# Performance work log

Hardware: AMD Instinct MI355X
Metric: run time of the kernel (lower is better)

The kernel has to match this reference:

```python
import jax, jax.numpy as jnp
import numpy as np

N_NODES = 100000
N_EDGES = 1600000
N_FEAT = 16
HIDDEN = 128
N_GRAPHS = 512


def setup_inputs() -> dict:
    key = jax.random.key(0)
    ks = jax.random.split(key, 9)
    x = jax.random.normal(ks[0], (N_NODES, N_FEAT), dtype=jnp.float32)
    edge_index = jax.random.randint(ks[1], (2, N_EDGES), 0, N_NODES, dtype=jnp.int64)
    batch = jnp.sort(jax.random.randint(ks[2], (N_NODES,), 0, N_GRAPHS, dtype=jnp.int64))
    s1 = 1.0 / np.sqrt(N_FEAT)
    s2 = 1.0 / np.sqrt(HIDDEN)
    W1 = jax.random.uniform(ks[3], (N_FEAT, HIDDEN), jnp.float32, -s1, s1)
    b1 = jax.random.uniform(ks[4], (HIDDEN,), jnp.float32, -s1, s1)
    W2 = jax.random.uniform(ks[5], (HIDDEN, HIDDEN), jnp.float32, -s2, s2)
    b2 = jax.random.uniform(ks[6], (HIDDEN,), jnp.float32, -s2, s2)
    Wl = jax.random.uniform(ks[7], (HIDDEN, 1), jnp.float32, -s2, s2)
    bl = jax.random.uniform(ks[8], (1,), jnp.float32, -s2, s2)
    return {"x": x, "edge_index": edge_index, "batch": batch,
            "W1": W1, "b1": b1, "W2": W2, "b2": b2, "Wl": Wl, "bl": bl}


def _gcn_conv(x, W, b, src, dst, n_nodes):
    # PyG GCNConv: h = x @ W; add self-loops; sym-normalized scatter-add; + bias
    h = x @ W  # [N, H]
    deg = jnp.zeros((n_nodes,), h.dtype).at[dst].add(1.0) + 1.0  # self-loop adds 1
    dinv = jax.lax.rsqrt(deg)  # deg >= 1, safe
    norm = dinv[src] * dinv[dst]  # [E]
    out = jnp.zeros_like(h).at[dst].add(h[src] * norm[:, None])
    out = out + h * (dinv * dinv)[:, None]  # self-loop term
    return out + b


def reference(x, edge_index, batch, W1, b1, W2, b2, Wl, bl):
    src, dst = edge_index[0], edge_index[1]
    n = x.shape[0]
    h = jax.nn.relu(_gcn_conv(x, W1, b1, src, dst, n))
    h = jax.nn.relu(_gcn_conv(h, W2, b2, src, dst, n))
    # global_mean_pool over graphs
    sums = jax.ops.segment_sum(h, batch, num_segments=N_GRAPHS)
    counts = jax.ops.segment_sum(jnp.ones((n,), h.dtype), batch, num_segments=N_GRAPHS)
    pooled = sums / jnp.maximum(counts, 1.0)[:, None]  # [G, H]
    return (pooled @ Wl + bl).squeeze(-1)  # [G]
```

## Files before the change

kernel.cpp:

```cpp
#include <hip/hip_runtime.h>
#include <hip/hip_bf16.h>

#define N_NODES 100000
#define N_EDGES 1600000
#define N_FEAT  16
#define HIDDEN  128
#define N_GRAPHS 512
#define CAP     64
#define NBKT    782
#define BN      128
#define CAPB    2560
#define EPB     4000

typedef unsigned short ushort_t;
typedef unsigned char uchar_t;
typedef short v8s __attribute__((ext_vector_type(8)));
typedef float v4f __attribute__((ext_vector_type(4)));
typedef float v2f __attribute__((ext_vector_type(2)));

#if defined(__has_builtin)
#if __has_builtin(__builtin_amdgcn_cvt_pk_f32_fp8) && __has_builtin(__builtin_amdgcn_cvt_pk_fp8_f32)
#define FP8_HW 1
#endif
#endif

__device__ __forceinline__ ushort_t f2bf(float f) {
    __hip_bfloat16 b = __float2bfloat16(f);
    return *(ushort_t*)&b;
}
__device__ __forceinline__ float bf_lo(unsigned u) {
    union { unsigned i; float f; } c; c.i = u << 16; return c.f;
}
__device__ __forceinline__ float bf_hi(unsigned u) {
    union { unsigned i; float f; } c; c.i = u & 0xffff0000u; return c.f;
}

__device__ __forceinline__ uchar_t f2fp8(float v) {
#ifdef FP8_HW
    return (uchar_t)(__builtin_amdgcn_cvt_pk_fp8_f32(v, 0.0f, 0, false) & 0xff);
#else
    if (!(v > 0.0f)) return 0;
    if (v >= 448.0f) return 0x7E;
    union { float f; unsigned u; } c; c.f = v;
    int e = ((c.u >> 23) & 255) - 127;
    unsigned m = c.u & 0x7fffff;
    if (e >= -6) {
        unsigned mm = m >> 20;
        unsigned rest = m & 0xfffff;
        if (rest > 0x80000u || (rest == 0x80000u && (mm & 1))) mm++;
        if (mm == 8) { mm = 0; e++; if (e > 8) return 0x7E; }
        return (uchar_t)(((e + 7) << 3) | mm);
    } else {
        int q = (int)(v * 512.0f + 0.5f);
        if (q > 7) q = 7;
        return (uchar_t)q;
    }
#endif
}

#ifndef FP8_HW
__device__ __forceinline__ float fp8d(unsigned b) {
    b &= 0xff;
    unsigned s = b >> 7, e = (b >> 3) & 15, m = b & 7;
    float v;
    if (e == 0) v = (float)m * (1.0f / 512.0f);
    else { union { unsigned u; float f; } c; c.u = ((e + 120u) << 23) | (m << 20); v = c.f; }
    return s ? -v : v;
}
#endif

__device__ __forceinline__ void fp8x8_acc(uint2 v, float& a0, float& a1, float& a2, float& a3,
                                          float& a4, float& a5, float& a6, float& a7) {
#ifdef FP8_HW
    v2f p0 = __builtin_amdgcn_cvt_pk_f32_fp8(v.x, false);
    v2f p1 = __builtin_amdgcn_cvt_pk_f32_fp8(v.x, true);
    v2f p2 = __builtin_amdgcn_cvt_pk_f32_fp8(v.y, false);
    v2f p3 = __builtin_amdgcn_cvt_pk_f32_fp8(v.y, true);
    a0 += p0[0]; a1 += p0[1]; a2 += p1[0]; a3 += p1[1];
    a4 += p2[0]; a5 += p2[1]; a6 += p3[0]; a7 += p3[1];
#else
    a0 += fp8d(v.x);       a1 += fp8d(v.x >> 8);
    a2 += fp8d(v.x >> 16); a3 += fp8d(v.x >> 24);
    a4 += fp8d(v.y);       a5 += fp8d(v.y >> 8);
    a6 += fp8d(v.y >> 16); a7 += fp8d(v.y >> 24);
#endif
}


__global__ __launch_bounds__(256) void k_part(const int* __restrict__ src,
                                              const int* __restrict__ dst,
                                              int* __restrict__ bcnt,
                                              int* __restrict__ ebuf,
                                              const float* __restrict__ W2,
                                              ushort_t* __restrict__ Bp) {
    int tid = threadIdx.x;

    if (blockIdx.x >= N_EDGES / EPB) {
        int idx = (blockIdx.x - N_EDGES / EPB) * 256 + tid;
        int j = idx & 7;
        int lane = (idx >> 3) & 63;
        int nt = (idx >> 9) & 7;
        int kt = idx >> 12;
        int k = kt * 32 + (lane >> 4) * 8 + j;
        int n = nt * 16 + (lane & 15);
        Bp[idx] = f2bf(W2[k * HIDDEN + n]);
        return;
    }

    __shared__ int h[NBKT];
    __shared__ int base[NBKT];
    __shared__ int r[NBKT];
    int e0 = blockIdx.x * EPB;

    for (int i = tid; i < NBKT; i += 256) { h[i] = 0; r[i] = 0; }
    __syncthreads();

    int nloc = (tid < EPB - 15 * 256) ? 16 : 15;
    int v[16], bb[16];
    #pragma unroll
    for (int k = 0; k < 16; ++k) {
        if (k < nloc) {
            int i = e0 + tid + k * 256;
            int s = src[i], d = dst[i];
            bb[k] = d >> 7;
            v[k] = s | ((d & 127) << 17);
            atomicAdd(&h[bb[k]], 1);
        }
    }
    __syncthreads();

    for (int i = tid; i < NBKT; i += 256)
        base[i] = atomicAdd(&bcnt[i], h[i]);
    __syncthreads();

    #pragma unroll
    for (int k = 0; k < 16; ++k) {
        if (k < nloc) {
            int b = bb[k];
            int pos = base[b] + atomicAdd(&r[b], 1);
            if (pos < CAPB) ebuf[b * CAPB + pos] = v[k];
        }
    }
}


__global__ __launch_bounds__(256) void k_fill(const int* __restrict__ bcnt,
                                              const int* __restrict__ ebuf,
                                              const float* __restrict__ x,
                                              int* __restrict__ esrc64,
                                              int* __restrict__ cnt,
                                              float* __restrict__ dinv,
                                              ushort_t* __restrict__ xb,
                                              uchar_t* __restrict__ h1q) {
    __shared__ int lcnt[BN];
    int tid = threadIdx.x;
    int b = blockIdx.x;
    int node0 = b << 7;

    if (tid < BN) lcnt[tid] = 0;
    __syncthreads();

    int nE = bcnt[b]; nE = nE > CAPB ? CAPB : nE;
    const int* eb = ebuf + b * CAPB;
    for (int i = tid; i < nE; i += 256) {
        int v = eb[i];
        int dl = v >> 17;
        int p = atomicAdd(&lcnt[dl], 1);
        if (p < CAP) esrc64[((node0 + dl) << 6) + p] = v & 0x1FFFF;
    }
    __syncthreads();

    if (tid < BN) {
        int node = node0 + tid;
        if (node < N_NODES) {
            int c = lcnt[tid];
            cnt[node] = c;
            dinv[node] = rsqrtf((float)c + 1.0f);
            int cc = c > CAP ? CAP : c;
            int pad = (cc + 7) & ~7;
            for (int p = cc; p < pad; ++p)
                esrc64[(node << 6) + p] = N_NODES;
        }
    }

    for (int i = tid; i < BN * N_FEAT; i += 256) {
        int nl = i >> 4;
        int node = node0 + nl;
        if (node < N_NODES) {
            float di = rsqrtf((float)lcnt[nl] + 1.0f);
            xb[node * N_FEAT + (i & 15)] = f2bf(x[node * N_FEAT + (i & 15)] * di);
        }
    }

    if (b == 0) {
        if (tid < N_FEAT) xb[N_NODES * N_FEAT + tid] = 0;
        if (tid < HIDDEN) h1q[(size_t)N_NODES * HIDDEN + tid] = 0;
    }
}


__global__ __launch_bounds__(256) void k_agg1f(const int* __restrict__ cnt,
                                               const int* __restrict__ esrc64,
                                               const float* __restrict__ dinv,
                                               const ushort_t* __restrict__ xb,
                                               const float* __restrict__ W1,
                                               const float* __restrict__ b1,
                                               uchar_t* __restrict__ h1q) {
    __shared__ float sw[N_FEAT * HIDDEN];
    __shared__ float sx[32][20];
    __shared__ float sdd[32];
    int tid = threadIdx.x;
    for (int i = tid; i < N_FEAT * HIDDEN; i += 256) sw[i] = W1[i];

    int wv = tid >> 6;
    int sub = (tid >> 3) & 7;
    int l8 = tid & 7;
    int nl = wv * 8 + sub;
    int node = blockIdx.x * 32 + nl;
    const unsigned* xr = (const unsigned*)xb;

    int deg = cnt[node]; deg = deg > CAP ? CAP : deg;
    int deg8 = (deg + 7) & ~7;
    int base = node << 6;
    float dd = dinv[node];

    float a0 = 0.0f, a1 = 0.0f;
    for (int j = 0; j < deg8; j += 8) {
        int4 ia = *(const int4*)(esrc64 + base + j);
        int4 ib = *(const int4*)(esrc64 + base + j + 4);
        unsigned u0 = xr[(unsigned)ia.x * 8 + l8];
        unsigned u1 = xr[(unsigned)ia.y * 8 + l8];
        unsigned u2 = xr[(unsigned)ia.z * 8 + l8];
        unsigned u3 = xr[(unsigned)ia.w * 8 + l8];
        unsigned u4 = xr[(unsigned)ib.x * 8 + l8];
        unsigned u5 = xr[(unsigned)ib.y * 8 + l8];
        unsigned u6 = xr[(unsigned)ib.z * 8 + l8];
        unsigned u7 = xr[(unsigned)ib.w * 8 + l8];
        a0 += bf_lo(u0) + bf_lo(u1) + bf_lo(u2) + bf_lo(u3)
            + bf_lo(u4) + bf_lo(u5) + bf_lo(u6) + bf_lo(u7);
        a1 += bf_hi(u0) + bf_hi(u1) + bf_hi(u2) + bf_hi(u3)
            + bf_hi(u4) + bf_hi(u5) + bf_hi(u6) + bf_hi(u7);
    }
    unsigned su = xr[(unsigned)node * 8 + l8];
    a0 = (a0 + bf_lo(su)) * dd;
    a1 = (a1 + bf_hi(su)) * dd;

    sx[nl][2 * l8] = a0;
    sx[nl][2 * l8 + 1] = a1;
    if (l8 == 0) sdd[nl] = dd;
    __syncthreads();

    int f = tid & 127, half = tid >> 7;
    float bias = b1[f];
    float acc[16];
    #pragma unroll
    for (int n = 0; n < 16; ++n) acc[n] = bias;
    #pragma unroll
    for (int k4 = 0; k4 < 4; ++k4) {
        float w0 = sw[(k4 * 4 + 0) * HIDDEN + f];
        float w1 = sw[(k4 * 4 + 1) * HIDDEN + f];
        float w2 = sw[(k4 * 4 + 2) * HIDDEN + f];
        float w3 = sw[(k4 * 4 + 3) * HIDDEN + f];
        #pragma unroll
        for (int n = 0; n < 16; ++n) {
            float4 xv = *(const float4*)(&sx[half * 16 + n][k4 * 4]);
            acc[n] += xv.x * w0 + xv.y * w1 + xv.z * w2 + xv.w * w3;
        }
    }
    int n0 = blockIdx.x * 32 + half * 16;
    #pragma unroll
    for (int n = 0; n < 16; ++n)
        h1q[(size_t)(n0 + n) * HIDDEN + f] =
            f2fp8(sdd[half * 16 + n] * fmaxf(acc[n], 0.0f));
}


__global__ __launch_bounds__(256) void k_l2(const int* __restrict__ cnt,
                                            const int* __restrict__ esrc64,
                                            const float* __restrict__ dinv,
                                            const uchar_t* __restrict__ h1q,
                                            const ushort_t* __restrict__ Bp,
                                            const float* __restrict__ b2,
                                            const float* __restrict__ Wl,
                                            float* __restrict__ snode) {
    __shared__ ushort_t sA[64 * 132];
    int tid = threadIdx.x;
    int wv = tid >> 6, lane = tid & 63;
    int l16 = lane & 15, q = lane >> 4;
    int node0 = blockIdx.x * 64;
    const uint2* h2 = (const uint2*)h1q;

    for (int p = 0; p < 4; ++p) {
        int nl = wv * 16 + p * 4 + q;
        int nodeIdx = node0 + nl;
        int node = nodeIdx < N_NODES ? nodeIdx : 0;
        int deg = cnt[node]; deg = deg > CAP ? CAP : deg;
        int deg8 = (deg + 7) & ~7;
        int base = node << 6;
        float dd = dinv[node];
        float a0 = 0.f, a1 = 0.f, a2 = 0.f, a3 = 0.f;
        float a4 = 0.f, a5 = 0.f, a6 = 0.f, a7 = 0.f;
        uint2 sv = h2[(unsigned)node * 16 + l16];
        fp8x8_acc(sv, a0, a1, a2, a3, a4, a5, a6, a7);

        int4 ia = *(const int4*)(esrc64 + base);
        int4 ib = *(const int4*)(esrc64 + base + 4);
        for (int j = 0; j < deg8; j += 8) {
            int jn = j + 8; jn = jn > CAP - 8 ? CAP - 8 : jn;
            int4 ian = *(const int4*)(esrc64 + base + jn);
            int4 ibn = *(const int4*)(esrc64 + base + jn + 4);
            uint2 v0 = h2[(unsigned)ia.x * 16 + l16];
            uint2 v1 = h2[(unsigned)ia.y * 16 + l16];
            uint2 v2 = h2[(unsigned)ia.z * 16 + l16];
            uint2 v3 = h2[(unsigned)ia.w * 16 + l16];
            uint2 v4 = h2[(unsigned)ib.x * 16 + l16];
            uint2 v5 = h2[(unsigned)ib.y * 16 + l16];
            uint2 v6 = h2[(unsigned)ib.z * 16 + l16];
            uint2 v7 = h2[(unsigned)ib.w * 16 + l16];
            fp8x8_acc(v0, a0, a1, a2, a3, a4, a5, a6, a7);
            fp8x8_acc(v1, a0, a1, a2, a3, a4, a5, a6, a7);
            fp8x8_acc(v2, a0, a1, a2, a3, a4, a5, a6, a7);
            fp8x8_acc(v3, a0, a1, a2, a3, a4, a5, a6, a7);
            fp8x8_acc(v4, a0, a1, a2, a3, a4, a5, a6, a7);
            fp8x8_acc(v5, a0, a1, a2, a3, a4, a5, a6, a7);
            fp8x8_acc(v6, a0, a1, a2, a3, a4, a5, a6, a7);
            fp8x8_acc(v7, a0, a1, a2, a3, a4, a5, a6, a7);
            ia = ian; ib = ibn;
        }
        unsigned r0 = (unsigned)f2bf(a0 * dd) | ((unsigned)f2bf(a1 * dd) << 16);
        unsigned r1 = (unsigned)f2bf(a2 * dd) | ((unsigned)f2bf(a3 * dd) << 16);
        unsigned r2 = (unsigned)f2bf(a4 * dd) | ((unsigned)f2bf(a5 * dd) << 16);
        unsigned r3 = (unsigned)f2bf(a6 * dd) | ((unsigned)f2bf(a7 * dd) << 16);
        uint2 w0; w0.x = r0; w0.y = r1;
        uint2 w1; w1.x = r2; w1.y = r3;
        *(uint2*)(&sA[nl * 132 + l16 * 8]) = w0;
        *(uint2*)(&sA[nl * 132 + l16 * 8 + 4]) = w1;
    }

    int m = lane & 15, quad = lane >> 4;
    const ushort_t* arow = &sA[(wv * 16 + m) * 132];

    v4f acc[8];
    #pragma unroll
    for (int nt = 0; nt < 8; ++nt) acc[nt] = (v4f){0.f, 0.f, 0.f, 0.f};

    #pragma unroll
    for (int kt = 0; kt < 4; ++kt) {
        union { v8s v; ushort4 q[2]; } au;
        au.q[0] = *(const ushort4*)(arow + kt * 32 + quad * 8);
        au.q[1] = *(const ushort4*)(arow + kt * 32 + quad * 8 + 4);
        #pragma unroll
        for (int nt = 0; nt < 8; ++nt) {
            v8s b = *(const v8s*)(Bp + ((kt * 8 + nt) * 64 + lane) * 8);
            acc[nt] = __builtin_amdgcn_mfma_f32_16x16x32_bf16(au.v, b, acc[nt], 0, 0, 0);
        }
    }

    float part[4] = {0, 0, 0, 0};
    #pragma unroll
    for (int nt = 0; nt < 8; ++nt) {
        float bb = b2[nt * 16 + m];
        float wl = Wl[nt * 16 + m];
        #pragma unroll
        for (int reg = 0; reg < 4; ++reg)
            part[reg] += fmaxf(acc[nt][reg] + bb, 0.0f) * wl;
    }
    int node0b = node0 + wv * 16;
    #pragma unroll
    for (int reg = 0; reg < 4; ++reg) {
        float p = part[reg];
        p += __shfl_xor(p, 1, 64);
        p += __shfl_xor(p, 2, 64);
        p += __shfl_xor(p, 4, 64);
        p += __shfl_xor(p, 8, 64);
        int node = node0b + quad * 4 + reg;
        if (m == 0 && node < N_NODES) snode[node] = p;
    }
}


__global__ __launch_bounds__(256) void k_pool(const float* __restrict__ snode,
                                              const int* __restrict__ batch,
                                              const float* __restrict__ bl,
                                              float* __restrict__ out) {
    int g = blockIdx.x;
    int tid = threadIdx.x;
    __shared__ float sred[4];

    int lo = 0, hi = N_NODES;
    while (lo < hi) { int mid = (lo + hi) >> 1; if (batch[mid] < g) lo = mid + 1; else hi = mid; }
    int start = lo;
    hi = N_NODES;
    while (lo < hi) { int mid = (lo + hi) >> 1; if (batch[mid] < g + 1) lo = mid + 1; else hi = mid; }
    int end = lo;

    float acc = 0.0f;
    for (int n = start + tid; n < end; n += 256) acc += snode[n];

    #pragma unroll
    for (int off = 32; off; off >>= 1) acc += __shfl_down(acc, off, 64);
    int wave = tid >> 6, lane = tid & 63;
    if (lane == 0) sred[wave] = acc;
    __syncthreads();
    if (tid == 0) {
        float s = sred[0] + sred[1] + sred[2] + sred[3];
        float cnt = (float)(end - start);
        out[g] = s / fmaxf(cnt, 1.0f) + bl[0];
    }
}


extern "C" void kernel_launch(void* const* d_in, const int* in_sizes, int n_in,
                              void* d_out, int out_size, void* d_ws, size_t ws_size,
                              hipStream_t stream) {
    const float* x    = (const float*)d_in[0];
    const int*   src  = (const int*)d_in[1];
    const int*   dst  = src + N_EDGES;
    const int*   batch= (const int*)d_in[2];
    const float* W1   = (const float*)d_in[3];
    const float* b1   = (const float*)d_in[4];
    const float* W2   = (const float*)d_in[5];
    const float* b2   = (const float*)d_in[6];
    const float* Wl   = (const float*)d_in[7];
    const float* bl   = (const float*)d_in[8];
    float* out = (float*)d_out;

    char* w = (char*)d_ws;
    size_t off = 0;
    auto alloc = [&](size_t bytes) { char* p = w + off; off = (off + bytes + 255) & ~(size_t)255; return p; };

    uchar_t* h1q   = (uchar_t*)alloc((size_t)(N_NODES + 1) * HIDDEN);
    int*   ebuf    = (int*)alloc((size_t)NBKT * CAPB * 4);
    ushort_t* xb   = (ushort_t*)alloc((size_t)(N_NODES + 1) * N_FEAT * 2);
    float* dinv    = (float*)alloc(N_NODES * 4);
    float* snode   = (float*)alloc(N_NODES * 4);
    int*   cnt     = (int*)alloc(N_NODES * 4);
    int*   esrc64  = (int*)alloc((size_t)N_NODES * CAP * 4);
    ushort_t* Bp   = (ushort_t*)alloc(16384 * 2);
    int*   bcnt    = (int*)alloc(NBKT * 4);

    hipMemsetAsync(bcnt, 0, NBKT * sizeof(int), stream);
    k_part<<<N_EDGES / EPB + 64, 256, 0, stream>>>(src, dst, bcnt, ebuf, W2, Bp);
    k_fill<<<NBKT, 256, 0, stream>>>(bcnt, ebuf, x, esrc64, cnt, dinv, xb, h1q);

    k_agg1f<<<N_NODES / 32, 256, 0, stream>>>(cnt, esrc64, dinv, xb, W1, b1, h1q);

    k_l2<<<(N_NODES + 63) / 64, 256, 0, stream>>>(cnt, esrc64, dinv, h1q, Bp, b2, Wl, snode);

    k_pool<<<N_GRAPHS, 256, 0, stream>>>(snode, batch, bl, out);
}
```

Before: 197.8 us.

## Build adjacency lists with direct global atomics instead of bucket partition pass

Replaces the two-pass bucketed edge partitioning (shared-memory histogram into per-bucket buffers, then per-bucket fill) with a single pass where each thread does a global atomicAdd on the per-node count and writes the source directly into the node's slot. This removes the intermediate ebuf traffic and one kernel's worth of reads. The trade is 1.6M uncoalesced global atomics and scattered writes instead of mostly local shared atomics, and a larger memset of the count array. The edge order within each node's list also becomes nondeterministic.

```diff
diff --git a/kernel.cpp b/kernel.cpp
--- a/kernel.cpp
+++ b/kernel.cpp
@@ -9,8 +9,7 @@
 #define CAP     64
 #define NBKT    782
 #define BN      128
-#define CAPB    2560
-#define EPB     4000
+#define NB_BUILD 1563
 
 typedef unsigned short ushort_t;
 typedef unsigned char uchar_t;
@@ -87,16 +86,16 @@
 }
 
 
-__global__ __launch_bounds__(256) void k_part(const int* __restrict__ src,
-                                              const int* __restrict__ dst,
-                                              int* __restrict__ bcnt,
-                                              int* __restrict__ ebuf,
-                                              const float* __restrict__ W2,
-                                              ushort_t* __restrict__ Bp) {
+__global__ __launch_bounds__(256) void k_build(const int* __restrict__ src,
+                                               const int* __restrict__ dst,
+                                               int* __restrict__ cnt,
+                                               int* __restrict__ esrc64,
+                                               const float* __restrict__ W2,
+                                               ushort_t* __restrict__ Bp) {
     int tid = threadIdx.x;
 
-    if (blockIdx.x >= N_EDGES / EPB) {
-        int idx = (blockIdx.x - N_EDGES / EPB) * 256 + tid;
+    if (blockIdx.x >= NB_BUILD) {
+        int idx = (blockIdx.x - NB_BUILD) * 256 + tid;
         int j = idx & 7;
         int lane = (idx >> 3) & 63;
         int nt = (idx >> 9) & 7;
@@ -107,89 +106,48 @@
         return;
     }
 
-    __shared__ int h[NBKT];
-    __shared__ int base[NBKT];
-    __shared__ int r[NBKT];
-    int e0 = blockIdx.x * EPB;
-
-    for (int i = tid; i < NBKT; i += 256) { h[i] = 0; r[i] = 0; }
-    __syncthreads();
-
-    int nloc = (tid < EPB - 15 * 256) ? 16 : 15;
-    int v[16], bb[16];
-    #pragma unroll
-    for (int k = 0; k < 16; ++k) {
-        if (k < nloc) {
-            int i = e0 + tid + k * 256;
-            int s = src[i], d = dst[i];
-            bb[k] = d >> 7;
-            v[k] = s | ((d & 127) << 17);
-            atomicAdd(&h[bb[k]], 1);
-        }
-    }
-    __syncthreads();
-
-    for (int i = tid; i < NBKT; i += 256)
-        base[i] = atomicAdd(&bcnt[i], h[i]);
-    __syncthreads();
-
-    #pragma unroll
-    for (int k = 0; k < 16; ++k) {
-        if (k < nloc) {
-            int b = bb[k];
-            int pos = base[b] + atomicAdd(&r[b], 1);
-            if (pos < CAPB) ebuf[b * CAPB + pos] = v[k];
-        }
-    }
-}
-
-
-__global__ __launch_bounds__(256) void k_fill(const int* __restrict__ bcnt,
-                                              const int* __restrict__ ebuf,
-                                              const float* __restrict__ x,
-                                              int* __restrict__ esrc64,
-                                              int* __restrict__ cnt,
-                                              float* __restrict__ dinv,
-                                              ushort_t* __restrict__ xb,
-                                              uchar_t* __restrict__ h1q) {
-    __shared__ int lcnt[BN];
+    int t = (blockIdx.x * 256 + tid) * 4;
+    if (t >= N_EDGES) return;
+    int4 s4 = *(const int4*)(src + t);
+    int4 d4 = *(const int4*)(dst + t);
+    int p0 = atomicAdd(&cnt[d4.x], 1); if (p0 < CAP) esrc64[(d4.x << 6) + p0] = s4.x;
+    int p1 = atomicAdd(&cnt[d4.y], 1); if (p1 < CAP) esrc64[(d4.y << 6) + p1] = s4.y;
+    int p2 = atomicAdd(&cnt[d4.z], 1); if (p2 < CAP) esrc64[(d4.z << 6) + p2] = s4.z;
+    int p3 = atomicAdd(&cnt[d4.w], 1); if (p3 < CAP) esrc64[(d4.w << 6) + p3] = s4.w;
+}
+
+
+__global__ __launch_bounds__(256) void k_prescale(const int* __restrict__ cnt,
+                                                  const float* __restrict__ x,
+                                                  int* __restrict__ esrc64,
+                                                  float* __restrict__ dinv,
+                                                  ushort_t* __restrict__ xb,
+                                                  uchar_t* __restrict__ h1q) {
+    __shared__ float sdi[BN];
     int tid = threadIdx.x;
     int b = blockIdx.x;
     int node0 = b << 7;
 
-    if (tid < BN) lcnt[tid] = 0;
-    __syncthreads();
-
-    int nE = bcnt[b]; nE = nE > CAPB ? CAPB : nE;
-    const int* eb = ebuf + b * CAPB;
-    for (int i = tid; i < nE; i += 256) {
-        int v = eb[i];
-        int dl = v >> 17;
-        int p = atomicAdd(&lcnt[dl], 1);
-        if (p < CAP) esrc64[((node0 + dl) << 6) + p] = v & 0x1FFFF;
-    }
-    __syncthreads();
-
     if (tid < BN) {
         int node = node0 + tid;
         if (node < N_NODES) {
-            int c = lcnt[tid];
-            cnt[node] = c;
-            dinv[node] = rsqrtf((float)c + 1.0f);
+            int c = cnt[node];
+            float di = rsqrtf((float)c + 1.0f);
+            dinv[node] = di;
+            sdi[tid] = di;
             int cc = c > CAP ? CAP : c;
             int pad = (cc + 7) & ~7;
             for (int p = cc; p < pad; ++p)
                 esrc64[(node << 6) + p] = N_NODES;
         }
     }
+    __syncthreads();
 
     for (int i = tid; i < BN * N_FEAT; i += 256) {
         int nl = i >> 4;
         int node = node0 + nl;
-        if (node < N_NODES) {
-            float di = rsqrtf((float)lcnt[nl] + 1.0f);
-            xb[node * N_FEAT + (i & 15)] = f2bf(x[node * N_FEAT + (i & 15)] * di);
-        }
+        if (node < N_NODES)
+            xb[node * N_FEAT + (i & 15)] = f2bf(x[node * N_FEAT + (i & 15)] * sdi[nl]);
     }
 
     if (b == 0) {
@@ -430,18 +388,16 @@
     auto alloc = [&](size_t bytes) { char* p = w + off; off = (off + bytes + 255) & ~(size_t)255; return p; };
 
     uchar_t* h1q   = (uchar_t*)alloc((size_t)(N_NODES + 1) * HIDDEN);
-    int*   ebuf    = (int*)alloc((size_t)NBKT * CAPB * 4);
     ushort_t* xb   = (ushort_t*)alloc((size_t)(N_NODES + 1) * N_FEAT * 2);
     float* dinv    = (float*)alloc(N_NODES * 4);
     float* snode   = (float*)alloc(N_NODES * 4);
     int*   cnt     = (int*)alloc(N_NODES * 4);
     int*   esrc64  = (int*)alloc((size_t)N_NODES * CAP * 4);
     ushort_t* Bp   = (ushort_t*)alloc(16384 * 2);
-    int*   bcnt    = (int*)alloc(NBKT * 4);
-
-    hipMemsetAsync(bcnt, 0, NBKT * sizeof(int), stream);
-    k_part<<<N_EDGES / EPB + 64, 256, 0, stream>>>(src, dst, bcnt, ebuf, W2, Bp);
-    k_fill<<<NBKT, 256, 0, stream>>>(bcnt, ebuf, x, esrc64, cnt, dinv, xb, h1q);
+
+    hipMemsetAsync(cnt, 0, N_NODES * sizeof(int), stream);
+    k_build<<<NB_BUILD + 64, 256, 0, stream>>>(src, dst, cnt, esrc64, W2, Bp);
+    k_prescale<<<NBKT, 256, 0, stream>>>(cnt, x, esrc64, dinv, xb, h1q);
 
     k_agg1f<<<N_NODES / 32, 256, 0, stream>>>(cnt, esrc64, dinv, xb, W1, b1, h1q);
 
```

After: 302.6 us. +53.0%, slower.
